# Kernel tuning notes

Hardware: AMD Instinct MI355X
Metric: run time of the kernel (lower is better)

The kernel has to match this reference:

```python
import jax, jax.numpy as jnp
import numpy as np

S_LEN = 8        # stride_length
LEVELS = 4       # corr_levels
RADIUS = 3       # corr_radius
CD = 2 * RADIUS + 1  # corr_dim = 7
PLANES = ((0, 1), (0, 2), (1, 2))  # itertools.combinations(range(3), 2)


def _bilinear(img, pts):
    # img: (C,H,W); pts: (...,2) normalized [-1,1], x->W, y->H; align_corners=True, border padding
    C, H, W = img.shape
    x = jnp.clip((pts[..., 0] + 1.0) * 0.5 * (W - 1), 0.0, W - 1.0)
    y = jnp.clip((pts[..., 1] + 1.0) * 0.5 * (H - 1), 0.0, H - 1.0)
    x0f = jnp.floor(x); y0f = jnp.floor(y)
    x0 = x0f.astype(jnp.int32); y0 = y0f.astype(jnp.int32)
    x1 = jnp.minimum(x0 + 1, W - 1); y1 = jnp.minimum(y0 + 1, H - 1)
    wx = x - x0f; wy = y - y0f
    return (img[:, y0, x0] * (1 - wy) * (1 - wx) + img[:, y0, x1] * (1 - wy) * wx
            + img[:, y1, x0] * wy * (1 - wx) + img[:, y1, x1] * wy * wx)


def _trilinear(vol, pts):
    # vol: (C,D,H,W); pts: (...,3) normalized, x->W, y->H, z->D; align_corners=True, border padding
    C, D, H, W = vol.shape
    x = jnp.clip((pts[..., 0] + 1.0) * 0.5 * (W - 1), 0.0, W - 1.0)
    y = jnp.clip((pts[..., 1] + 1.0) * 0.5 * (H - 1), 0.0, H - 1.0)
    z = jnp.clip((pts[..., 2] + 1.0) * 0.5 * (D - 1), 0.0, float(max(D - 1, 0)))
    x0f = jnp.floor(x); y0f = jnp.floor(y); z0f = jnp.floor(z)
    x0 = x0f.astype(jnp.int32); y0 = y0f.astype(jnp.int32); z0 = z0f.astype(jnp.int32)
    x1 = jnp.minimum(x0 + 1, W - 1); y1 = jnp.minimum(y0 + 1, H - 1); z1 = jnp.minimum(z0 + 1, D - 1)
    wx = x - x0f; wy = y - y0f; wz = z - z0f
    out = (vol[:, z0, y0, x0] * (1 - wz) * (1 - wy) * (1 - wx)
           + vol[:, z0, y0, x1] * (1 - wz) * (1 - wy) * wx
           + vol[:, z0, y1, x0] * (1 - wz) * wy * (1 - wx)
           + vol[:, z0, y1, x1] * (1 - wz) * wy * wx
           + vol[:, z1, y0, x0] * wz * (1 - wy) * (1 - wx)
           + vol[:, z1, y0, x1] * wz * (1 - wy) * wx
           + vol[:, z1, y1, x0] * wz * wy * (1 - wx)
           + vol[:, z1, y1, x1] * wz * wy * wx)
    return out


def setup_inputs():
    key = jax.random.key(0)
    ks = jax.random.split(key, 5)
    B, N, V, DLAT = 1, 256, 96, 128
    coords = jax.random.uniform(ks[0], (B, S_LEN, N, 3), jnp.float32) * (V - 1)
    coords_init = jax.random.uniform(ks[1], (B, N, 3), jnp.float32) * (V - 1)
    feature_planes = jax.random.normal(ks[2], (B * S_LEN, DLAT * 3, V, V), jnp.float32)
    w1 = jax.random.normal(ks[3], (CD ** 4, 384), jnp.float32) * 0.02
    b1 = jnp.zeros((384,), jnp.float32)
    w2 = jax.random.normal(ks[4], (384, 256), jnp.float32) * 0.05
    b2 = jnp.zeros((256,), jnp.float32)
    return dict(coords=coords, coords_init=coords_init, feature_planes=feature_planes,
                w1=w1, b1=b1, w2=w2, b2=b2)


def _forward(coords, coords_init, feature_planes, w1, b1, w2, b2):
    B, S, N, _ = coords.shape
    dt = coords.dtype
    off = jnp.arange(CD, dtype=dt) - RADIUS
    oc = jnp.stack(jnp.meshgrid(off, off, indexing='ij'), -1)        # (7,7,2) spatial offsets
    oc3 = jnp.concatenate([oc, jnp.zeros_like(oc[..., :1])], -1)     # (7,7,3) zero time offset
    # ---- init_levels: feature pyramid + initial track features ----
    fp = feature_planes  # ((B S), (D*3), V, V)
    fplevels, tflevels = [], []
    for i in range(LEVELS):
        if i > 0:
            bs, c, v, _ = fp.shape
            fp = fp.reshape(bs, c, v // 2, 2, v // 2, 2).mean(axis=(3, 5))  # avg_pool2d(2,2)
        bs, c, v, _ = fp.shape
        d = c // 3
        lev = fp.reshape(B, S, d, 3, v, v).transpose(0, 1, 2, 4, 5, 3)  # (B,S,d,v,v,planes)
        fplevels.append(lev)
        scale3 = jnp.array([v - 1, v - 1, S - 1], dt)
        # time coordinate = batch index (faithful to get_track_features t construction)
        t = jnp.broadcast_to(jnp.arange(B, dtype=dt)[:, None, None], (B, N, 1))
        tfs = []
        for k, (a, b2_) in enumerate(PLANES):
            c3 = jnp.concatenate([coords_init[..., (a, b2_)] / (2.0 ** i), t], -1)  # (B,N,3)
            reg = c3[:, None, None, :, :] + oc3[None, :, :, None, :]  # (B,7,7,N,3)
            g = reg * (2.0 / scale3) - 1.0
            vol = lev[..., k].transpose(0, 2, 1, 3, 4)  # (B,d,S,v,v)
            samp = jax.vmap(_trilinear)(vol, g)          # (B,d,7,7,N)
            tfs.append(samp.reshape(B, d, CD * CD, N).transpose(0, 2, 3, 1))  # (B,49,N,d)
        tflevels.append(jnp.stack(tfs, -1))  # (B,49,N,d,planes)
    # ---- get_corr_features: per-level 4D correlation volumes + corr_mlp ----
    outs = []
    for i in range(LEVELS):
        lev = fplevels[i]
        v = lev.shape[3]; d = lev.shape[2]
        scale2 = jnp.array([v - 1, v - 1], dt)
        acc = None
        for k, (a, b2_) in enumerate(PLANES):
            c2 = (coords[..., (a, b2_)] / (2.0 ** i)).reshape(B * S, N, 2)
            reg = c2[:, :, None, None, :] + oc[None, None, :, :, :]  # (BS,N,7,7,2)
            g = reg * (2.0 / scale2) - 1.0
            frames = lev[..., k].reshape(B * S, d, v, v)
            cf2 = jax.vmap(_bilinear)(frames, g)                     # (BS,d,N,7,7)
            cf2 = cf2.transpose(0, 2, 3, 4, 1).reshape(B, S, N, CD, CD, d)  # b s n h w d
            tf = tflevels[i][..., k].transpose(0, 2, 3, 1).reshape(B, N, d, CD, CD)  # b n d x y
            c4 = jnp.einsum('bsnhwd,bndxy->bsnhwxy', cf2, tf).reshape(B * S * N, CD ** 4)
            h = jax.nn.gelu(c4 @ w1 + b1, approximate=True)
            o = h @ w2 + b2
            acc = o if acc is None else acc + o
        outs.append(acc)
    return jnp.concatenate(outs, -1).reshape(B, S, N, LEVELS * w2.shape[1])


def reference(coords, coords_init, feature_planes, w1, b1, w2, b2):
    return _forward(coords, coords_init, feature_planes, w1, b1, w2, b2)
```

## Files before the change

kernel.cpp:

```cpp
#include <hip/hip_runtime.h>
#include <hip/hip_bf16.h>
#include <math.h>

#define NTRK 256
#define DLAT 128
#define CDIM 7
#define CD2  49
#define CD4  2401
#define NH1  384
#define NH2  256
#define LDK  2432
#define PITCHB 272

#define SZ_L0 ((size_t)3 * 8 * 96 * 96 * 128)
#define SZ_L1 ((size_t)3 * 8 * 48 * 48 * 128)
#define SZ_L2 ((size_t)3 * 8 * 24 * 24 * 128)
#define SZ_L3 ((size_t)3 * 8 * 12 * 12 * 128)
#define SZ_TF ((size_t)3 * NTRK * DLAT * CD2)

typedef __attribute__((ext_vector_type(8))) short short8;
typedef __attribute__((ext_vector_type(4))) float f32x4;
typedef __attribute__((ext_vector_type(4))) unsigned int u32x4;


__device__ __forceinline__ float b2f(unsigned short u) {
    union { unsigned int i; float f; } c;
    c.i = ((unsigned int)u) << 16;
    return c.f;
}
__device__ __forceinline__ unsigned int f2b(float x) {
    __hip_bfloat16 h = __float2bfloat16(x);
    return (unsigned int)(*(unsigned short*)&h);
}

__device__ __forceinline__ float gelu_tanh(float x) {
    float x2 = x * x;
    float p = x * fmaf(0.044715f, x2, 1.0f);
    float e = __expf(-1.5957691216f * p);
    return __fdividef(x, 1.0f + e);
}

__device__ __forceinline__ int plane_a(int k) { return (k == 2) ? 1 : 0; }
__device__ __forceinline__ int plane_b(int k) { return (k == 0) ? 1 : 2; }

__device__ __forceinline__ int lev_v(int lev) { return 96 >> lev; }
__device__ __forceinline__ size_t lev_off(int lev) {
    return (lev > 0 ? SZ_L0 : 0) + (lev > 1 ? SZ_L1 : 0) + (lev > 2 ? SZ_L2 : 0);
}

__device__ __forceinline__ void gload16(const void* g, void* l) {
    __builtin_amdgcn_global_load_lds(
        (const __attribute__((address_space(1))) unsigned int*)g,
        (__attribute__((address_space(3))) unsigned int*)l,
        16, 0, 0);
}


__global__ __launch_bounds__(256) void cvt_cl_kernel(const float* __restrict__ in,
                                                     __hip_bfloat16* __restrict__ out) {
    __shared__ unsigned int lds[64][97];
    const int b = blockIdx.x;
    const int y = b % 96;
    const int ks = b / 96;
    const int k = ks >> 3, s = ks & 7;
    const int tid = threadIdx.x;
    for (int idx = tid; idx < 64 * 24; idx += 256) {
        int d2 = idx / 24, x4 = (idx - d2 * 24) * 4;
        const float* rlo = in + (((size_t)s * 384 + (2 * d2) * 3 + k) * 96 + y) * 96 + x4;
        const float* rhi = in + (((size_t)s * 384 + (2 * d2 + 1) * 3 + k) * 96 + y) * 96 + x4;
        float4 lo = *(const float4*)rlo;
        float4 hi = *(const float4*)rhi;
        lds[d2][x4 + 0] = f2b(lo.x) | (f2b(hi.x) << 16);
        lds[d2][x4 + 1] = f2b(lo.y) | (f2b(hi.y) << 16);
        lds[d2][x4 + 2] = f2b(lo.z) | (f2b(hi.z) << 16);
        lds[d2][x4 + 3] = f2b(lo.w) | (f2b(hi.w) << 16);
    }
    __syncthreads();
    unsigned int* orow = (unsigned int*)((unsigned short*)out + ((size_t)ks * 96 + y) * 96 * 128);
    for (int idx = tid; idx < 96 * 16; idx += 256) {
        int x = idx >> 4, q = idx & 15;
        u32x4 r;
        r[0] = lds[4 * q + 0][x];
        r[1] = lds[4 * q + 1][x];
        r[2] = lds[4 * q + 2][x];
        r[3] = lds[4 * q + 3][x];
        *(u32x4*)(orow + x * 64 + q * 4) = r;
    }
}


__global__ __launch_bounds__(256) void pool_cl(const __hip_bfloat16* __restrict__ in,
                                               __hip_bfloat16* __restrict__ out,
                                               int vin, int total8) {
    int idx = blockIdx.x * 256 + threadIdx.x;
    if (idx >= total8) return;
    int vout = vin >> 1;
    int d8 = idx & 15;
    int t = idx >> 4;
    int x = t % vout; t /= vout;
    int y = t % vout; t /= vout;
    const unsigned short* base = (const unsigned short*)in
        + (((size_t)t * vin + 2 * y) * vin + 2 * x) * 128 + d8 * 8;
    short8 a = *(const short8*)(base);
    short8 bq = *(const short8*)(base + 128);
    short8 c = *(const short8*)(base + (size_t)vin * 128);
    short8 d = *(const short8*)(base + (size_t)vin * 128 + 128);
    short8 r;
    #pragma unroll
    for (int j = 0; j < 8; ++j) {
        float sum = b2f((unsigned short)a[j]) + b2f((unsigned short)bq[j])
                  + b2f((unsigned short)c[j]) + b2f((unsigned short)d[j]);
        r[j] = (short)f2b(0.25f * sum);
    }
    *(short8*)((unsigned short*)out + ((((size_t)t * vout + y) * vout + x)) * 128 + d8 * 8) = r;
}


__global__ __launch_bounds__(256) void tf_all(const __hip_bfloat16* __restrict__ levbase,
                                              const float* __restrict__ coords_init,
                                              __hip_bfloat16* __restrict__ tfb) {
    const int bid = blockIdx.x;
    const int lev = bid / 768;
    const int r0 = bid - lev * 768;
    const int g = (r0 & 7) * 96 + (r0 >> 3);
    const int k = g >> 8;
    const int n = g & 255;
    const int v = lev_v(lev);
    const float inv_scale = 1.f / (float)(1 << lev);
    const float vm1 = (float)(v - 1);
    float cx = coords_init[n * 3 + plane_a(k)] * inv_scale;
    float cy = coords_init[n * 3 + plane_b(k)] * inv_scale;
    const unsigned short* frame = (const unsigned short*)levbase + lev_off(lev)
        + (size_t)(k * 8) * v * v * 128;
    unsigned short* dst = (unsigned short*)tfb + (size_t)lev * SZ_TF
        + ((size_t)(k * NTRK + n)) * (DLAT * CD2);
    for (int idx = threadIdx.x; idx < CD2 * 16; idx += 256) {
        int xy = idx >> 4;
        int c8 = idx & 15;
        int i = xy / CDIM, j = xy % CDIM;
        float X = fminf(fmaxf(cx + (float)(i - 3), 0.f), vm1);
        float Y = fminf(fmaxf(cy + (float)(j - 3), 0.f), vm1);
        float xf = floorf(X), yf = floorf(Y);
        int x0 = (int)xf, y0 = (int)yf;
        int x1 = min(x0 + 1, v - 1), y1 = min(y0 + 1, v - 1);
        float wx = X - xf, wy = Y - yf;
        const unsigned short* r00 = frame + ((size_t)y0 * v + x0) * 128 + c8 * 8;
        const unsigned short* r01 = frame + ((size_t)y0 * v + x1) * 128 + c8 * 8;
        const unsigned short* r10 = frame + ((size_t)y1 * v + x0) * 128 + c8 * 8;
        const unsigned short* r11 = frame + ((size_t)y1 * v + x1) * 128 + c8 * 8;
        short8 a = *(const short8*)r00, bq = *(const short8*)r01;
        short8 c = *(const short8*)r10, d = *(const short8*)r11;
        float w00 = (1.f - wy) * (1.f - wx), w01 = (1.f - wy) * wx;
        float w10 = wy * (1.f - wx), w11 = wy * wx;
        short8 r;
        #pragma unroll
        for (int e = 0; e < 8; ++e) {
            float val = b2f((unsigned short)a[e]) * w00 + b2f((unsigned short)bq[e]) * w01
                      + b2f((unsigned short)c[e]) * w10 + b2f((unsigned short)d[e]) * w11;
            r[e] = (short)f2b(val);
        }
        *(short8*)(dst + xy * 128 + c8 * 8) = r;
    }
}


__global__ __launch_bounds__(256) void corr_all(const __hip_bfloat16* __restrict__ levbase,
                                                const float* __restrict__ coords,
                                                const __hip_bfloat16* __restrict__ tfb,
                                                __hip_bfloat16* __restrict__ c4b) {
    __shared__ __align__(16) char patch[64 * PITCHB];
    __shared__ __align__(16) char tfs[64 * PITCHB];
    __shared__ float wxs[8], wys[8];
    const int bid = blockIdx.x;
    const int lk = bid >> 8;
    const int n = bid & 255;
    const int lev = lk / 3;
    const int k = lk - lev * 3;
    const int v = lev_v(lev);
    const int vv = v * v;
    const float inv_scale = 1.f / (float)(1 << lev);
    const int tid = threadIdx.x;
    const float vm1 = (float)(v - 1);

    const short8* tfg = (const short8*)(tfb + (size_t)lev * SZ_TF
        + ((size_t)(k * NTRK + n)) * (DLAT * CD2));
    for (int idx = tid; idx < 784; idx += 256) {
        int row = idx >> 4, c16 = idx & 15;
        *(short8*)(tfs + row * PITCHB + c16 * 16) = tfg[idx];
    }

    const int hwb = tid / 49;
    const int xy  = tid - hwb * 49;
    const bool act = tid < 245;

    const unsigned short* fbase = (const unsigned short*)levbase + lev_off(lev)
        + (size_t)(k * 8) * vv * 128;
    const int w4 = tid >> 6, l = tid & 63;
    const int l15 = l & 15, l4 = l >> 4;

    const int c8 = tid & 15;
    const int posb = tid >> 4;

    float cxc, cyc; int fxc, fyc;
    short8 pre[4];

    auto CALC = [&](int s) {
        const int sn = s * 256 + n;
        cxc = coords[sn * 3 + plane_a(k)] * inv_scale;
        cyc = coords[sn * 3 + plane_b(k)] * inv_scale;
        fxc = (int)floorf(cxc);
        fyc = (int)floorf(cyc);
    };
    auto PREF = [&](int s) {
        const unsigned short* frame = fbase + (size_t)s * vv * 128;
        #pragma unroll
        for (int q = 0; q < 4; ++q) {
            int pos = posb + 16 * q;
            int px = pos & 7, py = pos >> 3;
            int gx = min(max(fxc + px - 3, 0), v - 1);
            int gy = min(max(fyc + py - 3, 0), v - 1);
            pre[q] = *(const short8*)(frame + ((size_t)gy * v + gx) * 128 + c8 * 8);
        }
    };

    CALC(0); PREF(0);
    for (int s = 0; s < 8; ++s) {
        const float cx = cxc, cy = cyc;
        const int fx = fxc, fy = fyc;
        if (tid < 7) {
            float X = fminf(fmaxf(cx + (float)(tid - 3), 0.f), vm1);
            int g = min(max(fx + tid - 3, 0), v - 1);
            wxs[tid] = X - (float)g;
            float Y = fminf(fmaxf(cy + (float)(tid - 3), 0.f), vm1);
            int gy_ = min(max(fy + tid - 3, 0), v - 1);
            wys[tid] = Y - (float)gy_;
        }
        #pragma unroll
        for (int q = 0; q < 4; ++q)
            *(short8*)(patch + (posb + 16 * q) * PITCHB + c8 * 16) = pre[q];
        __syncthreads();

        f32x4 acc[4];
        #pragma unroll
        for (int nt = 0; nt < 4; ++nt) acc[nt] = (f32x4){0.f, 0.f, 0.f, 0.f};
        #pragma unroll
        for (int ks = 0; ks < 4; ++ks) {
            short8 af = *(const short8*)(patch + (16 * w4 + l15) * PITCHB + ks * 64 + l4 * 16);
            #pragma unroll
            for (int nt = 0; nt < 4; ++nt) {
                short8 bf = *(const short8*)(tfs + (16 * nt + l15) * PITCHB + ks * 64 + l4 * 16);
                acc[nt] = __builtin_amdgcn_mfma_f32_16x16x32_bf16(af, bf, acc[nt], 0, 0, 0);
            }
        }
        if (s < 7) { CALC(s + 1); PREF(s + 1); }
        __syncthreads();

        {
            const int row0 = 16 * w4 + l4 * 4;
            #pragma unroll
            for (int nt = 0; nt < 4; ++nt) {
                int col = nt * 16 + l15;
                #pragma unroll
                for (int j = 0; j < 4; ++j)
                    *(float*)(patch + (row0 + j) * PITCHB + col * 4) = acc[nt][j];
            }
        }
        __syncthreads();

        unsigned short* crow = (unsigned short*)c4b + ((size_t)lk * 2048 + s * 256 + n) * LDK;
        if (act) {
            int h = 0, w = hwb;
            unsigned short* op = crow + tid;
            const char* colbase = patch + xy * 4;
            #pragma unroll
            for (int it = 0; it < 10; ++it) {
                if (h < 7) {
                    float wxv = wxs[h], wyv = wys[w];
                    const char* tap = colbase + (w * 8 + h) * PITCHB;
                    float p00 = *(const float*)(tap);
                    float p01 = *(const float*)(tap + PITCHB);
                    float p10 = *(const float*)(tap + 8 * PITCHB);
                    float p11 = *(const float*)(tap + 9 * PITCHB);
                    float a  = fmaf(wxv, p01 - p00, p00);
                    float bq = fmaf(wxv, p11 - p10, p10);
                    *op = (unsigned short)f2b(fmaf(wyv, bq - a, a));
                }
                w += 5; if (w >= 7) { w -= 7; h += 1; }
                op += 245;
            }
        }
        if (tid < LDK - CD4) crow[CD4 + tid] = 0;
        __syncthreads();
    }
}


__global__ __launch_bounds__(256) void prep_w1t(const float* __restrict__ w1,
                                                __hip_bfloat16* __restrict__ w1t) {
    __shared__ float t[64][65];
    const int kk0 = blockIdx.x * 64, n0 = blockIdx.y * 64;
    const int tid = threadIdx.x;
    for (int idx = tid; idx < 4096; idx += 256) {
        int r = idx >> 6, c = idx & 63;
        int kk = kk0 + r;
        t[r][c] = (kk < CD4) ? w1[(size_t)kk * NH1 + n0 + c] : 0.f;
    }
    __syncthreads();
    for (int idx = tid; idx < 4096; idx += 256) {
        int r = idx >> 6, c = idx & 63;
        w1t[(size_t)(n0 + r) * LDK + kk0 + c] = __float2bfloat16(t[c][r]);
    }
}

__global__ __launch_bounds__(256) void prep_w2t(const float* __restrict__ w2,
                                                __hip_bfloat16* __restrict__ w2t) {
    int idx = blockIdx.x * 256 + threadIdx.x;
    if (idx >= NH2 * NH1) return;
    int n = idx / NH1, j = idx - n * NH1;
    w2t[idx] = __float2bfloat16(w2[(size_t)j * NH2 + n]);
}


__global__ __launch_bounds__(256) void gemm1_all(
    const __hip_bfloat16* __restrict__ A,
    const __hip_bfloat16* __restrict__ Bt,
    const float* __restrict__ b1,
    __hip_bfloat16* __restrict__ H) {
    __shared__ __align__(16) char smem[16384];
    char* Asm = smem;
    char* Bsm = smem + 8192;
    const int m0 = blockIdx.x * 128, n0 = blockIdx.y * 128;
    const int tid = threadIdx.x;
    const int w = tid >> 6, l = tid & 63;
    const int wr = w >> 1, wc = w & 1;
    const int l15 = l & 15, l4 = l >> 4;
    f32x4 acc[4][4];
    #pragma unroll
    for (int m = 0; m < 4; ++m)
        #pragma unroll
        for (int n = 0; n < 4; ++n) acc[m][n] = (f32x4){0.f, 0.f, 0.f, 0.f};
    const char* Ag = (const char*)(A + (size_t)(m0 + (tid >> 2)) * LDK) + (tid & 3) * 16;
    const char* Bg = (const char*)(Bt + (size_t)(n0 + (tid >> 2)) * LDK) + (tid & 3) * 16;
    char* AsmW = Asm + w * 1024;
    char* BsmW = Bsm + w * 1024;
    for (int kb = 0; kb < LDK * 2; kb += 64) {
        gload16(Ag + kb, AsmW);
        gload16(Ag + (size_t)64 * LDK * 2 + kb, AsmW + 4096);
        gload16(Bg + kb, BsmW);
        gload16(Bg + (size_t)64 * LDK * 2 + kb, BsmW + 4096);
        __syncthreads();
        short8 af[4], bfr[4];
        #pragma unroll
        for (int m = 0; m < 4; ++m)
            af[m] = *(const short8*)(Asm + (wr * 64 + m * 16 + l15) * 64 + l4 * 16);
        #pragma unroll
        for (int n = 0; n < 4; ++n)
            bfr[n] = *(const short8*)(Bsm + (wc * 64 + n * 16 + l15) * 64 + l4 * 16);
        #pragma unroll
        for (int m = 0; m < 4; ++m)
            #pragma unroll
            for (int n = 0; n < 4; ++n)
                acc[m][n] = __builtin_amdgcn_mfma_f32_16x16x32_bf16(af[m], bfr[n], acc[m][n], 0, 0, 0);
        __syncthreads();
    }
    #pragma unroll
    for (int m = 0; m < 4; ++m) {
        int row = m0 + wr * 64 + m * 16 + l4 * 4;
        #pragma unroll
        for (int n = 0; n < 4; ++n) {
            int col = n0 + wc * 64 + n * 16 + l15;
            float bias = b1[col];
            #pragma unroll
            for (int j = 0; j < 4; ++j)
                H[(size_t)(row + j) * NH1 + col] = __float2bfloat16(gelu_tanh(acc[m][n][j] + bias));
        }
    }
}


__global__ __launch_bounds__(256) void gemm2_all(
    const __hip_bfloat16* __restrict__ Hin,
    const __hip_bfloat16* __restrict__ Bt,
    const float* __restrict__ b2,
    float* __restrict__ out) {
    __shared__ __align__(16) char smem[8192];
    char* Asm = smem;
    char* Bsm = smem + 4096;
    const int lev = blockIdx.x >> 5;
    const int m0 = (blockIdx.x & 31) * 64, n0 = blockIdx.y * 64;
    const int tid = threadIdx.x;
    const int w = tid >> 6, l = tid & 63;
    const int wr = w >> 1, wc = w & 1;
    const int l15 = l & 15, l4 = l >> 4;
    f32x4 acc[2][2];
    #pragma unroll
    for (int m = 0; m < 2; ++m)
        #pragma unroll
        for (int n = 0; n < 2; ++n) acc[m][n] = (f32x4){0.f, 0.f, 0.f, 0.f};
    const char* Bg = (const char*)(Bt + (size_t)(n0 + (tid >> 2)) * NH1) + (tid & 3) * 16;
    char* AsmW = Asm + w * 1024;
    char* BsmW = Bsm + w * 1024;
    for (int p = 0; p < 3; ++p) {
        const char* Ag = (const char*)(Hin
            + (size_t)((lev * 3 + p) * 2048 + m0 + (tid >> 2)) * NH1) + (tid & 3) * 16;
        for (int jb = 0; jb < NH1 * 2; jb += 64) {
            gload16(Ag + jb, AsmW);
            gload16(Bg + jb, BsmW);
            __syncthreads();
            short8 af[2], bfr[2];
            #pragma unroll
            for (int m = 0; m < 2; ++m)
                af[m] = *(const short8*)(Asm + (wr * 32 + m * 16 + l15) * 64 + l4 * 16);
            #pragma unroll
            for (int n = 0; n < 2; ++n)
                bfr[n] = *(const short8*)(Bsm + (wc * 32 + n * 16 + l15) * 64 + l4 * 16);
            #pragma unroll
            for (int m = 0; m < 2; ++m)
                #pragma unroll
                for (int n = 0; n < 2; ++n)
                    acc[m][n] = __builtin_amdgcn_mfma_f32_16x16x32_bf16(af[m], bfr[n], acc[m][n], 0, 0, 0);
            __syncthreads();
        }
    }
    #pragma unroll
    for (int m = 0; m < 2; ++m) {
        int row = m0 + wr * 32 + m * 16 + l4 * 4;
        #pragma unroll
        for (int n = 0; n < 2; ++n) {
            int col = n0 + wc * 32 + n * 16 + l15;
            float bias3 = 3.f * b2[col];
            #pragma unroll
            for (int j = 0; j < 4; ++j)
                out[(size_t)(row + j) * 1024 + lev * NH2 + col] = acc[m][n][j] + bias3;
        }
    }
}


extern "C" void kernel_launch(void* const* d_in, const int* in_sizes, int n_in,
                              void* d_out, int out_size, void* d_ws, size_t ws_size,
                              hipStream_t stream) {
    const float* coords      = (const float*)d_in[0];
    const float* coords_init = (const float*)d_in[1];
    const float* fp0         = (const float*)d_in[2];
    const float* w1          = (const float*)d_in[3];
    const float* b1          = (const float*)d_in[4];
    const float* w2          = (const float*)d_in[5];
    const float* b2          = (const float*)d_in[6];
    float* out = (float*)d_out;
    char* ws = (char*)d_ws;

    __hip_bfloat16* lev0 = (__hip_bfloat16*)ws;      ws += SZ_L0 * 2;
    __hip_bfloat16* lev1 = (__hip_bfloat16*)ws;      ws += SZ_L1 * 2;
    __hip_bfloat16* lev2 = (__hip_bfloat16*)ws;      ws += SZ_L2 * 2;
    __hip_bfloat16* lev3 = (__hip_bfloat16*)ws;      ws += SZ_L3 * 2;
    __hip_bfloat16* tfb  = (__hip_bfloat16*)ws;      ws += (size_t)4 * SZ_TF * 2;
    __hip_bfloat16* c4b  = (__hip_bfloat16*)ws;      ws += (size_t)24576 * LDK * 2;
    __hip_bfloat16* h_ws = (__hip_bfloat16*)ws;      ws += (size_t)24576 * NH1 * 2;
    __hip_bfloat16* w1t  = (__hip_bfloat16*)ws;      ws += (size_t)NH1 * LDK * 2;
    __hip_bfloat16* w2t  = (__hip_bfloat16*)ws;      ws += (size_t)NH2 * NH1 * 2;

    prep_w1t<<<dim3(38, 6), 256, 0, stream>>>(w1, w1t);
    prep_w2t<<<(NH2 * NH1 + 255) / 256, 256, 0, stream>>>(w2, w2t);

    cvt_cl_kernel<<<24 * 96, 256, 0, stream>>>(fp0, lev0);
    pool_cl<<<(int)((SZ_L1 / 8 + 255) / 256), 256, 0, stream>>>(lev0, lev1, 96, (int)(SZ_L1 / 8));
    pool_cl<<<(int)((SZ_L2 / 8 + 255) / 256), 256, 0, stream>>>(lev1, lev2, 48, (int)(SZ_L2 / 8));
    pool_cl<<<(int)((SZ_L3 / 8 + 255) / 256), 256, 0, stream>>>(lev2, lev3, 24, (int)(SZ_L3 / 8));

    tf_all<<<4 * 768, 256, 0, stream>>>(lev0, coords_init, tfb);
    corr_all<<<3072, 256, 0, stream>>>(lev0, coords, tfb, c4b);
    gemm1_all<<<dim3(192, 3), 256, 0, stream>>>(c4b, w1t, b1, h_ws);
    gemm2_all<<<dim3(128, 4), 256, 0, stream>>>(h_ws, w2t, b2, out);
}
```

Measured before the change: 260.0 us.

## Software-pipeline corr_all interpolation with separate correlation buffer and double-buffered weights

```diff
diff --git a/kernel.cpp b/kernel.cpp
--- a/kernel.cpp
+++ b/kernel.cpp
@@ -11,6 +11,7 @@
 #define NH2  256
 #define LDK  2432
 #define PITCHB 272
+#define CPITCH 272
 
 #define SZ_L0 ((size_t)3 * 8 * 96 * 96 * 128)
 #define SZ_L1 ((size_t)3 * 8 * 48 * 48 * 128)
@@ -170,7 +171,8 @@
                                                 __hip_bfloat16* __restrict__ c4b) {
     __shared__ __align__(16) char patch[64 * PITCHB];
     __shared__ __align__(16) char tfs[64 * PITCHB];
-    __shared__ float wxs[8], wys[8];
+    __shared__ __align__(16) char cbuf[64 * CPITCH];
+    __shared__ float wxs[2][8], wys[2][8];
     const int bid = blockIdx.x;
     const int lk = bid >> 8;
     const int n = bid & 255;
@@ -222,65 +224,22 @@
             pre[q] = *(const short8*)(frame + ((size_t)gy * v + gx) * 128 + c8 * 8);
         }
     };
-
-    CALC(0); PREF(0);
-    for (int s = 0; s < 8; ++s) {
-        const float cx = cxc, cy = cyc;
-        const int fx = fxc, fy = fyc;
-        if (tid < 7) {
-            float X = fminf(fmaxf(cx + (float)(tid - 3), 0.f), vm1);
-            int g = min(max(fx + tid - 3, 0), v - 1);
-            wxs[tid] = X - (float)g;
-            float Y = fminf(fmaxf(cy + (float)(tid - 3), 0.f), vm1);
-            int gy_ = min(max(fy + tid - 3, 0), v - 1);
-            wys[tid] = Y - (float)gy_;
-        }
-        #pragma unroll
-        for (int q = 0; q < 4; ++q)
-            *(short8*)(patch + (posb + 16 * q) * PITCHB + c8 * 16) = pre[q];
-        __syncthreads();
-
-        f32x4 acc[4];
-        #pragma unroll
-        for (int nt = 0; nt < 4; ++nt) acc[nt] = (f32x4){0.f, 0.f, 0.f, 0.f};
-        #pragma unroll
-        for (int ks = 0; ks < 4; ++ks) {
-            short8 af = *(const short8*)(patch + (16 * w4 + l15) * PITCHB + ks * 64 + l4 * 16);
-            #pragma unroll
-            for (int nt = 0; nt < 4; ++nt) {
-                short8 bf = *(const short8*)(tfs + (16 * nt + l15) * PITCHB + ks * 64 + l4 * 16);
-                acc[nt] = __builtin_amdgcn_mfma_f32_16x16x32_bf16(af, bf, acc[nt], 0, 0, 0);
-            }
-        }
-        if (s < 7) { CALC(s + 1); PREF(s + 1); }
-        __syncthreads();
-
-        {
-            const int row0 = 16 * w4 + l4 * 4;
-            #pragma unroll
-            for (int nt = 0; nt < 4; ++nt) {
-                int col = nt * 16 + l15;
-                #pragma unroll
-                for (int j = 0; j < 4; ++j)
-                    *(float*)(patch + (row0 + j) * PITCHB + col * 4) = acc[nt][j];
-            }
-        }
-        __syncthreads();
-
-        unsigned short* crow = (unsigned short*)c4b + ((size_t)lk * 2048 + s * 256 + n) * LDK;
+    auto INTERP = [&](int sp) {
+        unsigned short* crow = (unsigned short*)c4b + ((size_t)lk * 2048 + sp * 256 + n) * LDK;
+        const int p = sp & 1;
         if (act) {
             int h = 0, w = hwb;
             unsigned short* op = crow + tid;
-            const char* colbase = patch + xy * 4;
+            const char* colbase = cbuf + xy * 4;
             #pragma unroll
             for (int it = 0; it < 10; ++it) {
                 if (h < 7) {
-                    float wxv = wxs[h], wyv = wys[w];
-                    const char* tap = colbase + (w * 8 + h) * PITCHB;
+                    float wxv = wxs[p][h], wyv = wys[p][w];
+                    const char* tap = colbase + (w * 8 + h) * CPITCH;
                     float p00 = *(const float*)(tap);
-                    float p01 = *(const float*)(tap + PITCHB);
-                    float p10 = *(const float*)(tap + 8 * PITCHB);
-                    float p11 = *(const float*)(tap + 9 * PITCHB);
+                    float p01 = *(const float*)(tap + CPITCH);
+                    float p10 = *(const float*)(tap + 8 * CPITCH);
+                    float p11 = *(const float*)(tap + 9 * CPITCH);
                     float a  = fmaf(wxv, p01 - p00, p00);
                     float bq = fmaf(wxv, p11 - p10, p10);
                     *op = (unsigned short)f2b(fmaf(wyv, bq - a, a));
@@ -290,8 +249,50 @@
             }
         }
         if (tid < LDK - CD4) crow[CD4 + tid] = 0;
+    };
+
+    CALC(0); PREF(0);
+    for (int s = 0; s < 8; ++s) {
+        #pragma unroll
+        for (int q = 0; q < 4; ++q)
+            *(short8*)(patch + (posb + 16 * q) * PITCHB + c8 * 16) = pre[q];
+        if (tid < 7) {
+            float X = fminf(fmaxf(cxc + (float)(tid - 3), 0.f), vm1);
+            int g = min(max(fxc + tid - 3, 0), v - 1);
+            wxs[s & 1][tid] = X - (float)g;
+            float Y = fminf(fmaxf(cyc + (float)(tid - 3), 0.f), vm1);
+            int gy_ = min(max(fyc + tid - 3, 0), v - 1);
+            wys[s & 1][tid] = Y - (float)gy_;
+        }
+        if (s > 0) INTERP(s - 1);
         __syncthreads();
-    }
+
+        f32x4 acc[4];
+        #pragma unroll
+        for (int nt = 0; nt < 4; ++nt) acc[nt] = (f32x4){0.f, 0.f, 0.f, 0.f};
+        #pragma unroll
+        for (int ks = 0; ks < 4; ++ks) {
+            short8 af = *(const short8*)(patch + (16 * w4 + l15) * PITCHB + ks * 64 + l4 * 16);
+            #pragma unroll
+            for (int nt = 0; nt < 4; ++nt) {
+                short8 bf = *(const short8*)(tfs + (16 * nt + l15) * PITCHB + ks * 64 + l4 * 16);
+                acc[nt] = __builtin_amdgcn_mfma_f32_16x16x32_bf16(af, bf, acc[nt], 0, 0, 0);
+            }
+        }
+        if (s < 7) { CALC(s + 1); PREF(s + 1); }
+        {
+            const int row0 = 16 * w4 + l4 * 4;
+            #pragma unroll
+            for (int nt = 0; nt < 4; ++nt) {
+                int col = nt * 16 + l15;
+                #pragma unroll
+                for (int j = 0; j < 4; ++j)
+                    *(float*)(cbuf + (row0 + j) * CPITCH + col * 4) = acc[nt][j];
+            }
+        }
+        __syncthreads();
+    }
+    INTERP(7);
 }
 
 
```

Result: no change. 262.0 us (+0.8%).
